# Kernel tuning notes

Measured on AMD Instinct MI355X. Metric: run time of the kernel, lower is better.

The kernel has to match this reference:

```python
import jax, jax.numpy as jnp
import numpy as np

Q = 3  # q_order: SelfONN concatenates powers x^1..x^Q on channel dim

def selfonn_conv(x, w, b, pad):
    # x: (B, C, H, W); w: (O, C*Q, kh, kw); b: (O,)
    xp = jnp.concatenate([x ** (i + 1) for i in range(Q)], axis=1)
    y = jax.lax.conv_general_dilated(
        xp, w, window_strides=(1, 1), padding=[(pad, pad), (pad, pad)],
        dimension_numbers=("NCHW", "OIHW", "NCHW"))
    return y + b[None, :, None, None]

def setup_inputs() -> dict:
    key = jax.random.key(0)
    ks = jax.random.split(key, 9)
    B, C, H, W = 4, 64, 64, 64
    P = 64  # pab_channels
    s1 = 1.0 / np.sqrt(C * Q)          # 1x1 convs
    s3 = 1.0 / np.sqrt(C * Q * 9)      # 3x3 convs
    return {
        "x": jax.random.normal(ks[0], (B, C, H, W), jnp.float32),
        "top_w": jax.random.normal(ks[1], (P, C * Q, 1, 1), jnp.float32) * s1,
        "top_b": jnp.zeros((P,), jnp.float32),
        "center_w": jax.random.normal(ks[2], (P, C * Q, 1, 1), jnp.float32) * s1,
        "center_b": jnp.zeros((P,), jnp.float32),
        "bottom_w": jax.random.normal(ks[3], (C, C * Q, 3, 3), jnp.float32) * s3,
        "bottom_b": jnp.zeros((C,), jnp.float32),
        "out_w": jax.random.normal(ks[4], (C, C * Q, 3, 3), jnp.float32) * s3,
        "out_b": jnp.zeros((C,), jnp.float32),
    }

def reference(x, top_w, top_b, center_w, center_b, bottom_w, bottom_b, out_w, out_b):
    B, C, H, W = x.shape
    HW = H * W
    x_top = selfonn_conv(x, top_w, top_b, 0).reshape(B, -1, HW)            # (B, P, HW)
    x_center = selfonn_conv(x, center_w, center_b, 0).reshape(B, -1, HW)  # (B, P, HW)
    x_bottom = selfonn_conv(x, bottom_w, bottom_b, 1).reshape(B, C, HW)   # (B, C, HW)
    x_center = jnp.swapaxes(x_center, 1, 2)  # (B, HW, P)
    x_bottom = jnp.swapaxes(x_bottom, 1, 2)  # (B, HW, C)
    sp = jnp.einsum("bnp,bpm->bnm", x_center, x_top)  # (B, HW, HW)
    # GLOBAL softmax over the entire HW*HW map per sample (dim=1 on flattened view)
    sp = jax.nn.softmax(sp.reshape(B, -1), axis=1).reshape(B, HW, HW)
    sp = jnp.einsum("bnm,bmc->bnc", sp, x_bottom)  # (B, HW, C)
    # faithful to torch: raw reshape (B, HW, C) -> (B, C, H, W), no transpose
    sp = sp.reshape(B, C, H, W)
    return selfonn_conv(x + sp, out_w, out_b, 1)
```

## Files before the change

### kernel.cpp

```cpp
#include <hip/hip_runtime.h>
#include <hip/hip_bf16.h>

namespace {
constexpr int IMG    = 262144;
constexpr int MS     = 4;
constexpr int PADIMG = 4356;
constexpr float LOG2E = 1.44269504088896340736f;
constexpr int WBFO  = 0;
constexpr int XPADO = 122880;
constexpr int TOPO  = 1795584;
constexpr int CENO  = 2319872;
constexpr int BOTO  = 2844160;
constexpr int PVO   = 3368448;
constexpr int MSO   = 5465600;
constexpr int ZSO   = 5467648;
}

using half8v  = __attribute__((ext_vector_type(8))) _Float16;
using half4v  = __attribute__((ext_vector_type(4))) _Float16;
using short8v = __attribute__((ext_vector_type(8))) short;
typedef __attribute__((ext_vector_type(4))) float f32x4;

__device__ __forceinline__ short f2bf(float f) {
    __hip_bfloat16 h = __float2bfloat16(f);
    return *reinterpret_cast<short*>(&h);
}
__device__ __forceinline__ float bf2f(short s) {
    unsigned u = ((unsigned)(unsigned short)s) << 16;
    return __uint_as_float(u);
}

__global__ __launch_bounds__(256) void k_prep(const float* __restrict__ bw, const float* __restrict__ ow,
                                              const float* __restrict__ tw, const float* __restrict__ cw,
                                              _Float16* __restrict__ wbf,
                                              const float* __restrict__ x, _Float16* __restrict__ xpad) {
    __shared__ float xs[64 * 65];
    int bx = blockIdx.x, t = threadIdx.x;
    if (bx < 960) {
        int idx = bx * 256 + t;
        if (idx < 221184) {
            int tsel = idx / 110592;
            int r    = idx - tsel * 110592;
            int tap  = r / 12288;
            int rr   = r - tap * 12288;
            int ck   = rr / 2048;
            int r2   = rr - ck * 2048;
            int o    = r2 >> 5;
            int ki   = r2 & 31;
            int k    = ck * 32 + ki;
            int p    = k >> 6, ci = k & 63;
            const float* src = tsel ? ow : bw;
            wbf[idx] = (_Float16)src[o * 1728 + (p * 64 + ci) * 9 + tap];
        } else {
            int j = idx - 221184;
            int tsel = j / 12288;
            int rr   = j - tsel * 12288;
            int ck   = rr / 2048;
            int r2   = rr - ck * 2048;
            int o    = r2 >> 5;
            int ki   = r2 & 31;
            int k    = ck * 32 + ki;
            wbf[idx] = (_Float16)(tsel ? cw[o * 192 + k] * LOG2E : tw[o * 192 + k]);
        }
        return;
    }
    int bx2 = bx - 960;
    int b = bx2 >> 6, h = bx2 & 63;
    {
        _Float16* base = xpad + (size_t)b * 6 * PADIMG * 32;
        int px[6];
        px[0] = (h + 1) * 66;
        px[1] = (h + 1) * 66 + 65;
        px[2] = h;
        px[3] = 65 * 66 + h;
        int npx = 4;
        if (h < 2) { px[4] = 64 + h; px[5] = 65 * 66 + 64 + h; npx = 6; }
        int pi = t / 24, ck = t % 24;
        if (pi < npx) {
            int cp = ck >> 2, q = ck & 3;
            half8v z = {0, 0, 0, 0, 0, 0, 0, 0};
            *(half8v*)&base[((size_t)cp * PADIMG + px[pi]) * 32 + q * 8] = z;
        }
    }
    #pragma unroll
    for (int it = 0; it < 16; ++it) {
        int idx = it * 256 + t;
        int ci = idx >> 6, wc = idx & 63;
        xs[ci * 65 + wc] = x[b * IMG + ci * 4096 + h * 64 + wc];
    }
    __syncthreads();
    _Float16* dst = xpad + ((size_t)b * 6 * PADIMG + (h + 1) * 66 + 1) * 32;
    #pragma unroll
    for (int it = 0; it < 6; ++it) {
        int u = it * 256 + t;
        int ck = u >> 8, within = u & 255;
        int px = within >> 2, q = within & 3;
        int k0 = ck * 32 + q * 8;
        int p = k0 >> 6, c0 = k0 & 63;
        half8v o;
        #pragma unroll
        for (int j = 0; j < 8; ++j) {
            float v = xs[(c0 + j) * 65 + px];
            float pw = (p == 0) ? v : ((p == 1) ? v * v : v * v * v);
            o[j] = (_Float16)pw;
        }
        *(half8v*)&dst[((size_t)ck * PADIMG + px) * 32 + q * 8] = o;
    }
}

__device__ __forceinline__ void conv3d32(int bx, int t,
                                         const _Float16* __restrict__ src,
                                         const _Float16* __restrict__ wt,
                                         const float* __restrict__ bias,
                                         _Float16* __restrict__ dh_, float* __restrict__ df) {
    int lane = t & 63, w = t >> 6;
    int l16 = lane & 15, quad = lane >> 4;
    int oh = bx >> 8, mt = bx & 255;
    int b = mt >> 6, h = mt & 63;
    const _Float16* abase = src + ((size_t)b * 6 * PADIMG + (h + 1) * 66 + 1 + w * 16 + l16) * 32 + quad * 8;
    const _Float16* bbase = wt + (size_t)(oh * 32 + l16) * 32 + quad * 8;
    f32x4 acc[2];
    acc[0] = (f32x4){0.f, 0.f, 0.f, 0.f};
    acc[1] = (f32x4){0.f, 0.f, 0.f, 0.f};
    for (int tap = 0; tap < 9; ++tap) {
        int dh = tap / 3 - 1, dw = tap % 3 - 1;
        const _Float16* arow = abase + (dh * 66 + dw) * 32;
        const _Float16* brow = bbase + (size_t)tap * 6 * 2048;
        #pragma unroll
        for (int c6 = 0; c6 < 6; ++c6) {
            half8v afr  = *(const half8v*)&arow[(size_t)c6 * PADIMG * 32];
            half8v bfr0 = *(const half8v*)&brow[(size_t)c6 * 2048];
            half8v bfr1 = *(const half8v*)&brow[(size_t)c6 * 2048 + 512];
            acc[0] = __builtin_amdgcn_mfma_f32_16x16x32_f16(afr, bfr0, acc[0], 0, 0, 0);
            acc[1] = __builtin_amdgcn_mfma_f32_16x16x32_f16(afr, bfr1, acc[1], 0, 0, 0);
        }
    }
    #pragma unroll
    for (int nf = 0; nf < 2; ++nf) {
        int c = oh * 32 + nf * 16 + l16;
        float bv = bias[c];
        size_t oi = (size_t)b * 262144 + (size_t)c * 4096 + h * 64 + w * 16 + quad * 4;
        if (dh_) {
            half4v o;
            #pragma unroll
            for (int r = 0; r < 4; ++r) o[r] = (_Float16)(acc[nf][r] + bv);
            *(half4v*)&dh_[oi] = o;
        } else {
            float4 o = make_float4(acc[nf][0] + bv, acc[nf][1] + bv, acc[nf][2] + bv, acc[nf][3] + bv);
            *(float4*)&df[oi] = o;
        }
    }
}

__global__ __launch_bounds__(256) void k_convs(const _Float16* __restrict__ xpad,
                                               const _Float16* __restrict__ wbf,
                                               const float* __restrict__ tb, const float* __restrict__ cb,
                                               const float* __restrict__ bbias,
                                               _Float16* __restrict__ topd, _Float16* __restrict__ cend,
                                               _Float16* __restrict__ botb) {
    int bx = blockIdx.x, t = threadIdx.x;
    if (bx < 512) {
        conv3d32(bx, t, xpad, wbf , bbias, botb, nullptr);
        return;
    }
    int bx2 = bx - 512;
    int lane = t & 63, w = t >> 6;
    int l16 = lane & 15, quad = lane >> 4;
    int ot = bx2 >> 8, mt = bx2 & 255;
    int b = mt >> 6, h = mt & 63;
    const _Float16* wt   = wbf + (ot ? 233472 : 221184);
    const float*    bias = ot ? cb : tb;
    _Float16*       dst  = (ot ? cend : topd) + (size_t)b * IMG;
    const _Float16* abase = xpad + ((size_t)b * 6 * PADIMG + (h + 1) * 66 + 1 + w * 16 + l16) * 32 + quad * 8;
    const _Float16* bbase = wt + (size_t)l16 * 32 + quad * 8;
    f32x4 acc[4];
    #pragma unroll
    for (int nf = 0; nf < 4; ++nf) acc[nf] = (f32x4){0.f, 0.f, 0.f, 0.f};
    #pragma unroll
    for (int kc = 0; kc < 6; ++kc) {
        half8v afr = *(const half8v*)&abase[(size_t)kc * PADIMG * 32];
        #pragma unroll
        for (int nf = 0; nf < 4; ++nf) {
            half8v bfr = *(const half8v*)&bbase[(size_t)kc * 2048 + nf * 16 * 32];
            acc[nf] = __builtin_amdgcn_mfma_f32_16x16x32_f16(afr, bfr, acc[nf], 0, 0, 0);
        }
    }
    _Float16* dp = dst + (size_t)(h * 64 + w * 16) * 64;
    #pragma unroll
    for (int nf = 0; nf < 4; ++nf) {
        float bv = bias[nf * 16 + l16];
        if (ot) bv *= LOG2E;
        #pragma unroll
        for (int r = 0; r < 4; ++r)
            dp[(quad * 4 + r) * 64 + nf * 16 + l16] = (_Float16)(acc[nf][r] + bv);
    }
}

__global__ __launch_bounds__(256) void k_attn(float* __restrict__ ws) {
    __shared__ _Float16 ltop[64 * 72];
    __shared__ _Float16 lbot[64 * 72];
    __shared__ _Float16 lp[128 * 72];
    int t    = threadIdx.x;
    int lane = t & 63, w = t >> 6;
    int l16  = lane & 15, quad = lane >> 4;
    int bx = blockIdx.x;
    int st = bx & 31, b = (bx >> 5) & 3, s = bx >> 7;
    int n0 = st * 128;
    const _Float16* topg = (const _Float16*)(ws + TOPO) + (size_t)b * IMG;
    const _Float16* ceng = (const _Float16*)(ws + CENO) + (size_t)b * IMG;
    const _Float16* botg = (const _Float16*)(ws + BOTO) + (size_t)b * IMG;

    half8v afr[2][2];
    #pragma unroll
    for (int i = 0; i < 2; ++i)
        #pragma unroll
        for (int kk = 0; kk < 2; ++kk)
            afr[i][kk] = *(const half8v*)&ceng[(size_t)(n0 + w * 32 + i * 16 + l16) * 64 + kk * 32 + quad * 8];

    int r0 = t >> 3, r1 = r0 + 32, off = (t & 7) * 8;
    int q2 = quad >> 1;
    int lpw = (w * 32 + quad * 4) * 72;
    int lpr = (w * 32 + l16) * 72;
    int rb3 = (l16 >> 3) & 1;

    f32x4 pv[2][4];
    #pragma unroll
    for (int i = 0; i < 2; ++i)
        #pragma unroll
        for (int j = 0; j < 4; ++j) pv[i][j] = (f32x4){0.f, 0.f, 0.f, 0.f};
    float runm = -3.0e38f, zacc = 0.f;

    int mp = s * 1024;
    half8v rt0 = *(const half8v*)&topg[(size_t)(mp + r0) * 64 + off];
    half8v rt1 = *(const half8v*)&topg[(size_t)(mp + r1) * 64 + off];
    half8v rb0 = *(const half8v*)&botg[(size_t)r0 * 4096 + mp + off];
    half8v rb1 = *(const half8v*)&botg[(size_t)r1 * 4096 + mp + off];

    for (int tt = 0; tt < 16; ++tt) {
        __syncthreads();
        *(half8v*)&ltop[r0 * 72 + off] = rt0;
        *(half8v*)&ltop[r1 * 72 + off] = rt1;
        *(half8v*)&lbot[r0 * 72 + off] = rb0;
        *(half8v*)&lbot[r1 * 72 + off] = rb1;
        __syncthreads();
        if (tt < 15) {
            int m1 = s * 1024 + (tt + 1) * 64;
            rt0 = *(const half8v*)&topg[(size_t)(m1 + r0) * 64 + off];
            rt1 = *(const half8v*)&topg[(size_t)(m1 + r1) * 64 + off];
            rb0 = *(const half8v*)&botg[(size_t)r0 * 4096 + m1 + off];
            rb1 = *(const half8v*)&botg[(size_t)r1 * 4096 + m1 + off];
        }
        f32x4 sa[2][4];
        #pragma unroll
        for (int i = 0; i < 2; ++i)
            #pragma unroll
            for (int j = 0; j < 4; ++j) sa[i][j] = (f32x4){0.f, 0.f, 0.f, 0.f};
        #pragma unroll
        for (int kk = 0; kk < 2; ++kk)
            #pragma unroll
            for (int j = 0; j < 4; ++j) {
                half8v bfr = *(half8v*)&ltop[(j * 16 + l16) * 72 + kk * 32 + quad * 8];
                sa[0][j] = __builtin_amdgcn_mfma_f32_16x16x32_f16(afr[0][kk], bfr, sa[0][j], 0, 0, 0);
                sa[1][j] = __builtin_amdgcn_mfma_f32_16x16x32_f16(afr[1][kk], bfr, sa[1][j], 0, 0, 0);
            }
        float tm = -3.0e38f;
        #pragma unroll
        for (int i = 0; i < 2; ++i)
            #pragma unroll
            for (int j = 0; j < 4; ++j)
                #pragma unroll
                for (int r = 0; r < 4; ++r) tm = fmaxf(tm, sa[i][j][r]);
        for (int o2 = 32; o2; o2 >>= 1) tm = fmaxf(tm, __shfl_xor(tm, o2, 64));
        float newm = fmaxf(runm, tm);
        if (newm > runm) {
            float sc = exp2f(runm - newm);
            zacc *= sc;
            #pragma unroll
            for (int i = 0; i < 2; ++i)
                #pragma unroll
                for (int j = 0; j < 4; ++j) pv[i][j] *= sc;
            runm = newm;
        }
        #pragma unroll
        for (int i = 0; i < 2; ++i)
            #pragma unroll
            for (int j = 0; j < 4; ++j) {
                int cb = (j ^ q2) * 16 + l16;
                #pragma unroll
                for (int r = 0; r < 4; ++r) {
                    float e = exp2f(sa[i][j][r] - runm);
                    zacc += e;
                    lp[lpw + i * 1152 + r * 72 + cb] = (_Float16)e;
                }
            }
        half8v pa[2][2];
        #pragma unroll
        for (int i = 0; i < 2; ++i)
            #pragma unroll
            for (int kk = 0; kk < 2; ++kk) {
                int jj = kk * 2 + q2;
                pa[i][kk] = *(half8v*)&lp[lpr + i * 1152 + ((jj ^ rb3) * 16) + (quad & 1) * 8];
            }
        #pragma unroll
        for (int kk = 0; kk < 2; ++kk)
            #pragma unroll
            for (int j = 0; j < 4; ++j) {
                half8v bb = *(half8v*)&lbot[(j * 16 + l16) * 72 + kk * 32 + quad * 8];
                pv[0][j] = __builtin_amdgcn_mfma_f32_16x16x32_f16(pa[0][kk], bb, pv[0][j], 0, 0, 0);
                pv[1][j] = __builtin_amdgcn_mfma_f32_16x16x32_f16(pa[1][kk], bb, pv[1][j], 0, 0, 0);
            }
    }
    for (int o2 = 32; o2; o2 >>= 1) zacc += __shfl_xor(zacc, o2, 64);
    if (lane == 0) {
        ws[MSO + s * 512 + b * 128 + st * 4 + w] = runm;
        ws[ZSO + s * 512 + b * 128 + st * 4 + w] = zacc;
    }
    short* pvp = (short*)(ws + PVO) + (size_t)s * 1048576 + (size_t)b * IMG;
    #pragma unroll
    for (int i = 0; i < 2; ++i)
        #pragma unroll
        for (int j = 0; j < 4; ++j)
            #pragma unroll
            for (int r = 0; r < 4; ++r)
                pvp[(size_t)(n0 + w * 32 + i * 16 + quad * 4 + r) * 64 + j * 16 + l16] = f2bf(pv[i][j][r]);
}

__global__ __launch_bounds__(256) void k_finalu(const float* __restrict__ x, float* __restrict__ ws,
                                                _Float16* __restrict__ upad) {
    __shared__ float us[64 * 65];
    __shared__ float rm[4], rz[4];
    int t = threadIdx.x, bx = blockIdx.x;
    int b = bx >> 6, h = bx & 63;
    int g = t & 127;
    float mv[4];
    float m = -3.0e38f;
    #pragma unroll
    for (int s = 0; s < 4; ++s) {
        mv[s] = ws[MSO + s * 512 + b * 128 + g];
        m = fmaxf(m, mv[s]);
    }
    for (int o2 = 32; o2; o2 >>= 1) m = fmaxf(m, __shfl_xor(m, o2, 64));
    if ((t & 63) == 0) rm[t >> 6] = m;
    __syncthreads();
    float M = fmaxf(fmaxf(rm[0], rm[1]), fmaxf(rm[2], rm[3]));
    float z = 0.f;
    if (t < 128) {
        #pragma unroll
        for (int s = 0; s < 4; ++s)
            z += ws[ZSO + s * 512 + b * 128 + g] * exp2f(mv[s] - M);
    }
    for (int o2 = 32; o2; o2 >>= 1) z += __shfl_xor(z, o2, 64);
    if ((t & 63) == 0) rz[t >> 6] = z;
    __syncthreads();
    float Z = rz[0] + rz[1] + rz[2] + rz[3];

    const short* pvb = (const short*)(ws + PVO) + (size_t)b * IMG;
    int hg = h >> 5;
    #pragma unroll
    for (int it = 0; it < 2; ++it) {
        int idx = it * 2048 + t * 8;
        int ci = idx >> 6, wc = idx & 63;
        int rem = ci * 4096 + h * 64 + wc;
        int grp = ci * 2 + hg;
        float acc[8] = {};
        #pragma unroll
        for (int s = 0; s < MS; ++s) {
            float scl = exp2f(ws[MSO + s * 512 + b * 128 + grp] - M);
            short8v pvv = *(const short8v*)&pvb[(size_t)s * 1048576 + rem];
            #pragma unroll
            for (int i = 0; i < 8; ++i) acc[i] += bf2f(pvv[i]) * scl;
        }
        float4 x0 = *(const float4*)&x[(size_t)b * IMG + rem];
        float4 x1 = *(const float4*)&x[(size_t)b * IMG + rem + 4];
        float xv[8] = {x0.x, x0.y, x0.z, x0.w, x1.x, x1.y, x1.z, x1.w};
        #pragma unroll
        for (int i = 0; i < 8; ++i)
            us[ci * 65 + wc + i] = xv[i] + acc[i] / Z;
    }
    __syncthreads();
    _Float16* dst = upad + ((size_t)b * 6 * PADIMG + (h + 1) * 66 + 1) * 32;
    #pragma unroll
    for (int it = 0; it < 6; ++it) {
        int u = it * 256 + t;
        int ck = u >> 8, within = u & 255;
        int px = within >> 2, q = within & 3;
        int k0 = ck * 32 + q * 8;
        int p = k0 >> 6, c0 = k0 & 63;
        half8v o;
        #pragma unroll
        for (int j = 0; j < 8; ++j) {
            float v = us[(c0 + j) * 65 + px];
            float pw = (p == 0) ? v : ((p == 1) ? v * v : v * v * v);
            o[j] = (_Float16)pw;
        }
        *(half8v*)&dst[((size_t)ck * PADIMG + px) * 32 + q * 8] = o;
    }
}

__global__ __launch_bounds__(256) void k_conv3o(const _Float16* __restrict__ upad,
                                                const _Float16* __restrict__ wout,
                                                const float* __restrict__ ob,
                                                float* __restrict__ out) {
    conv3d32(blockIdx.x, threadIdx.x, upad, wout, ob, nullptr, out);
}

extern "C" void kernel_launch(void* const* d_in, const int* in_sizes, int n_in,
                              void* d_out, int out_size, void* d_ws, size_t ws_size,
                              hipStream_t stream) {
    (void)in_sizes; (void)n_in; (void)out_size; (void)ws_size;
    const float* x  = (const float*)d_in[0];
    const float* tw = (const float*)d_in[1];
    const float* tb = (const float*)d_in[2];
    const float* cw = (const float*)d_in[3];
    const float* cb = (const float*)d_in[4];
    const float* bw = (const float*)d_in[5];
    const float* bb = (const float*)d_in[6];
    const float* ow = (const float*)d_in[7];
    const float* ob = (const float*)d_in[8];
    float* ws  = (float*)d_ws;
    float* out = (float*)d_out;

    _Float16* wbf  = (_Float16*)(ws + WBFO);
    _Float16* wout = wbf + 110592;
    _Float16* xpad = (_Float16*)(ws + XPADO);
    _Float16* topb = (_Float16*)(ws + TOPO);
    _Float16* cenb = (_Float16*)(ws + CENO);
    _Float16* botb = (_Float16*)(ws + BOTO);

    hipLaunchKernelGGL(k_prep, dim3(1216), dim3(256), 0, stream, bw, ow, tw, cw, wbf, x, xpad);
    hipLaunchKernelGGL(k_convs, dim3(1024), dim3(256), 0, stream, xpad, wbf, tb, cb, bb, topb, cenb, botb);
    hipLaunchKernelGGL(k_attn, dim3(512), dim3(256), 0, stream, ws);
    hipLaunchKernelGGL(k_finalu, dim3(256), dim3(256), 0, stream, x, ws, xpad);
    hipLaunchKernelGGL(k_conv3o, dim3(512), dim3(256), 0, stream, xpad, wout, ob, out);
}
```

Baseline: 167.0 us.

## Split attention key range across up to 8 slices with grid swizzle and MFMA priority

Makes the number of key splits in the flash-style attention kernel a runtime parameter, raising it from 4 to 8 when the workspace is large enough. This doubles the attention grid to fill more CUs, at the cost of more partial results to merge. The attention block index is also swizzled across XCDs, MFMA sections are wrapped in s_setprio, and the libm exp2f calls are replaced with the hardware exp2 builtin. The finalize kernel moves to 512 threads to merge the extra partials and multiplies by a reciprocal instead of dividing.

```diff
diff --git a/kernel.cpp b/kernel.cpp
--- a/kernel.cpp
+++ b/kernel.cpp
@@ -3,7 +3,6 @@
 
 namespace {
 constexpr int IMG    = 262144;
-constexpr int MS     = 4;
 constexpr int PADIMG = 4356;
 constexpr float LOG2E = 1.44269504088896340736f;
 constexpr int WBFO  = 0;
@@ -12,8 +11,9 @@
 constexpr int CENO  = 2319872;
 constexpr int BOTO  = 2844160;
 constexpr int PVO   = 3368448;
-constexpr int MSO   = 5465600;
-constexpr int ZSO   = 5467648;
+constexpr int MSO4  = 5465600;
+constexpr int MSO8  = 7562752;
+constexpr size_t NEED8 = (size_t)(MSO8 + 8192) * 4;
 }
 
 using half8v  = __attribute__((ext_vector_type(8))) _Float16;
@@ -196,16 +196,18 @@
     }
 }
 
-__global__ __launch_bounds__(256) void k_attn(float* __restrict__ ws) {
+__global__ __launch_bounds__(256) void k_attn(float* __restrict__ ws, int mtiles, int msoOff, int zsoOff) {
     __shared__ _Float16 ltop[64 * 72];
     __shared__ _Float16 lbot[64 * 72];
     __shared__ _Float16 lp[128 * 72];
     int t    = threadIdx.x;
     int lane = t & 63, w = t >> 6;
     int l16  = lane & 15, quad = lane >> 4;
-    int bx = blockIdx.x;
+    int bxr = blockIdx.x;
+    int bx  = (bxr & 7) * ((int)gridDim.x >> 3) + (bxr >> 3);
     int st = bx & 31, b = (bx >> 5) & 3, s = bx >> 7;
     int n0 = st * 128;
+    int mbase = s * mtiles * 64;
     const _Float16* topg = (const _Float16*)(ws + TOPO) + (size_t)b * IMG;
     const _Float16* ceng = (const _Float16*)(ws + CENO) + (size_t)b * IMG;
     const _Float16* botg = (const _Float16*)(ws + BOTO) + (size_t)b * IMG;
@@ -230,21 +232,20 @@
         for (int j = 0; j < 4; ++j) pv[i][j] = (f32x4){0.f, 0.f, 0.f, 0.f};
     float runm = -3.0e38f, zacc = 0.f;
 
-    int mp = s * 1024;
-    half8v rt0 = *(const half8v*)&topg[(size_t)(mp + r0) * 64 + off];
-    half8v rt1 = *(const half8v*)&topg[(size_t)(mp + r1) * 64 + off];
-    half8v rb0 = *(const half8v*)&botg[(size_t)r0 * 4096 + mp + off];
-    half8v rb1 = *(const half8v*)&botg[(size_t)r1 * 4096 + mp + off];
-
-    for (int tt = 0; tt < 16; ++tt) {
+    half8v rt0 = *(const half8v*)&topg[(size_t)(mbase + r0) * 64 + off];
+    half8v rt1 = *(const half8v*)&topg[(size_t)(mbase + r1) * 64 + off];
+    half8v rb0 = *(const half8v*)&botg[(size_t)r0 * 4096 + mbase + off];
+    half8v rb1 = *(const half8v*)&botg[(size_t)r1 * 4096 + mbase + off];
+
+    for (int tt = 0; tt < mtiles; ++tt) {
         __syncthreads();
         *(half8v*)&ltop[r0 * 72 + off] = rt0;
         *(half8v*)&ltop[r1 * 72 + off] = rt1;
         *(half8v*)&lbot[r0 * 72 + off] = rb0;
         *(half8v*)&lbot[r1 * 72 + off] = rb1;
         __syncthreads();
-        if (tt < 15) {
-            int m1 = s * 1024 + (tt + 1) * 64;
+        if (tt < mtiles - 1) {
+            int m1 = mbase + (tt + 1) * 64;
             rt0 = *(const half8v*)&topg[(size_t)(m1 + r0) * 64 + off];
             rt1 = *(const half8v*)&topg[(size_t)(m1 + r1) * 64 + off];
             rb0 = *(const half8v*)&botg[(size_t)r0 * 4096 + m1 + off];
@@ -255,6 +256,7 @@
         for (int i = 0; i < 2; ++i)
             #pragma unroll
             for (int j = 0; j < 4; ++j) sa[i][j] = (f32x4){0.f, 0.f, 0.f, 0.f};
+        __builtin_amdgcn_s_setprio(1);
         #pragma unroll
         for (int kk = 0; kk < 2; ++kk)
             #pragma unroll
@@ -263,17 +265,20 @@
                 sa[0][j] = __builtin_amdgcn_mfma_f32_16x16x32_f16(afr[0][kk], bfr, sa[0][j], 0, 0, 0);
                 sa[1][j] = __builtin_amdgcn_mfma_f32_16x16x32_f16(afr[1][kk], bfr, sa[1][j], 0, 0, 0);
             }
+        __builtin_amdgcn_s_setprio(0);
         float tm = -3.0e38f;
         #pragma unroll
         for (int i = 0; i < 2; ++i)
             #pragma unroll
-            for (int j = 0; j < 4; ++j)
-                #pragma unroll
-                for (int r = 0; r < 4; ++r) tm = fmaxf(tm, sa[i][j][r]);
+            for (int j = 0; j < 4; ++j) {
+                float a = fmaxf(sa[i][j][0], sa[i][j][1]);
+                float c = fmaxf(sa[i][j][2], sa[i][j][3]);
+                tm = fmaxf(tm, fmaxf(a, c));
+            }
         for (int o2 = 32; o2; o2 >>= 1) tm = fmaxf(tm, __shfl_xor(tm, o2, 64));
         float newm = fmaxf(runm, tm);
         if (newm > runm) {
-            float sc = exp2f(runm - newm);
+            float sc = __builtin_amdgcn_exp2f(runm - newm);
             zacc *= sc;
             #pragma unroll
             for (int i = 0; i < 2; ++i)
@@ -288,7 +293,7 @@
                 int cb = (j ^ q2) * 16 + l16;
                 #pragma unroll
                 for (int r = 0; r < 4; ++r) {
-                    float e = exp2f(sa[i][j][r] - runm);
+                    float e = __builtin_amdgcn_exp2f(sa[i][j][r] - runm);
                     zacc += e;
                     lp[lpw + i * 1152 + r * 72 + cb] = (_Float16)e;
                 }
@@ -301,6 +306,7 @@
                 int jj = kk * 2 + q2;
                 pa[i][kk] = *(half8v*)&lp[lpr + i * 1152 + ((jj ^ rb3) * 16) + (quad & 1) * 8];
             }
+        __builtin_amdgcn_s_setprio(1);
         #pragma unroll
         for (int kk = 0; kk < 2; ++kk)
             #pragma unroll
@@ -309,11 +315,12 @@
                 pv[0][j] = __builtin_amdgcn_mfma_f32_16x16x32_f16(pa[0][kk], bb, pv[0][j], 0, 0, 0);
                 pv[1][j] = __builtin_amdgcn_mfma_f32_16x16x32_f16(pa[1][kk], bb, pv[1][j], 0, 0, 0);
             }
+        __builtin_amdgcn_s_setprio(0);
     }
     for (int o2 = 32; o2; o2 >>= 1) zacc += __shfl_xor(zacc, o2, 64);
     if (lane == 0) {
-        ws[MSO + s * 512 + b * 128 + st * 4 + w] = runm;
-        ws[ZSO + s * 512 + b * 128 + st * 4 + w] = zacc;
+        ws[msoOff + s * 512 + b * 128 + st * 4 + w] = runm;
+        ws[zsoOff + s * 512 + b * 128 + st * 4 + w] = zacc;
     }
     short* pvp = (short*)(ws + PVO) + (size_t)s * 1048576 + (size_t)b * IMG;
     #pragma unroll
@@ -325,47 +332,47 @@
                 pvp[(size_t)(n0 + w * 32 + i * 16 + quad * 4 + r) * 64 + j * 16 + l16] = f2bf(pv[i][j][r]);
 }
 
-__global__ __launch_bounds__(256) void k_finalu(const float* __restrict__ x, float* __restrict__ ws,
-                                                _Float16* __restrict__ upad) {
+__global__ __launch_bounds__(512) void k_finalu(const float* __restrict__ x, float* __restrict__ ws,
+                                                _Float16* __restrict__ upad,
+                                                int ms, int msoOff, int zsoOff) {
     __shared__ float us[64 * 65];
-    __shared__ float rm[4], rz[4];
+    __shared__ float rm[8], rz[8];
     int t = threadIdx.x, bx = blockIdx.x;
     int b = bx >> 6, h = bx & 63;
     int g = t & 127;
-    float mv[4];
     float m = -3.0e38f;
-    #pragma unroll
-    for (int s = 0; s < 4; ++s) {
-        mv[s] = ws[MSO + s * 512 + b * 128 + g];
-        m = fmaxf(m, mv[s]);
-    }
+    for (int s = 0; s < ms; ++s)
+        m = fmaxf(m, ws[msoOff + s * 512 + b * 128 + g]);
     for (int o2 = 32; o2; o2 >>= 1) m = fmaxf(m, __shfl_xor(m, o2, 64));
     if ((t & 63) == 0) rm[t >> 6] = m;
     __syncthreads();
-    float M = fmaxf(fmaxf(rm[0], rm[1]), fmaxf(rm[2], rm[3]));
+    float M = rm[0];
+    #pragma unroll
+    for (int j = 1; j < 8; ++j) M = fmaxf(M, rm[j]);
     float z = 0.f;
     if (t < 128) {
-        #pragma unroll
-        for (int s = 0; s < 4; ++s)
-            z += ws[ZSO + s * 512 + b * 128 + g] * exp2f(mv[s] - M);
+        for (int s = 0; s < ms; ++s)
+            z += ws[zsoOff + s * 512 + b * 128 + g] *
+                 __builtin_amdgcn_exp2f(ws[msoOff + s * 512 + b * 128 + g] - M);
     }
     for (int o2 = 32; o2; o2 >>= 1) z += __shfl_xor(z, o2, 64);
     if ((t & 63) == 0) rz[t >> 6] = z;
     __syncthreads();
-    float Z = rz[0] + rz[1] + rz[2] + rz[3];
+    float Z = 0.f;
+    #pragma unroll
+    for (int j = 0; j < 8; ++j) Z += rz[j];
+    float rZ = 1.0f / Z;
 
     const short* pvb = (const short*)(ws + PVO) + (size_t)b * IMG;
     int hg = h >> 5;
-    #pragma unroll
-    for (int it = 0; it < 2; ++it) {
-        int idx = it * 2048 + t * 8;
+    {
+        int idx = t * 8;
         int ci = idx >> 6, wc = idx & 63;
         int rem = ci * 4096 + h * 64 + wc;
         int grp = ci * 2 + hg;
         float acc[8] = {};
-        #pragma unroll
-        for (int s = 0; s < MS; ++s) {
-            float scl = exp2f(ws[MSO + s * 512 + b * 128 + grp] - M);
+        for (int s = 0; s < ms; ++s) {
+            float scl = __builtin_amdgcn_exp2f(ws[msoOff + s * 512 + b * 128 + grp] - M);
             short8v pvv = *(const short8v*)&pvb[(size_t)s * 1048576 + rem];
             #pragma unroll
             for (int i = 0; i < 8; ++i) acc[i] += bf2f(pvv[i]) * scl;
@@ -375,13 +382,13 @@
         float xv[8] = {x0.x, x0.y, x0.z, x0.w, x1.x, x1.y, x1.z, x1.w};
         #pragma unroll
         for (int i = 0; i < 8; ++i)
-            us[ci * 65 + wc + i] = xv[i] + acc[i] / Z;
+            us[ci * 65 + wc + i] = xv[i] + acc[i] * rZ;
     }
     __syncthreads();
     _Float16* dst = upad + ((size_t)b * 6 * PADIMG + (h + 1) * 66 + 1) * 32;
     #pragma unroll
-    for (int it = 0; it < 6; ++it) {
-        int u = it * 256 + t;
+    for (int it = 0; it < 3; ++it) {
+        int u = it * 512 + t;
         int ck = u >> 8, within = u & 255;
         int px = within >> 2, q = within & 3;
         int k0 = ck * 32 + q * 8;
@@ -407,7 +414,7 @@
 extern "C" void kernel_launch(void* const* d_in, const int* in_sizes, int n_in,
                               void* d_out, int out_size, void* d_ws, size_t ws_size,
                               hipStream_t stream) {
-    (void)in_sizes; (void)n_in; (void)out_size; (void)ws_size;
+    (void)in_sizes; (void)n_in; (void)out_size;
     const float* x  = (const float*)d_in[0];
     const float* tw = (const float*)d_in[1];
     const float* tb = (const float*)d_in[2];
@@ -427,9 +434,14 @@
     _Float16* cenb = (_Float16*)(ws + CENO);
     _Float16* botb = (_Float16*)(ws + BOTO);
 
+    int ms     = (ws_size >= NEED8) ? 8 : 4;
+    int mtiles = 64 / ms;
+    int msoOff = (ms == 8) ? MSO8 : MSO4;
+    int zsoOff = msoOff + ms * 512;
+
     hipLaunchKernelGGL(k_prep, dim3(1216), dim3(256), 0, stream, bw, ow, tw, cw, wbf, x, xpad);
     hipLaunchKernelGGL(k_convs, dim3(1024), dim3(256), 0, stream, xpad, wbf, tb, cb, bb, topb, cenb, botb);
-    hipLaunchKernelGGL(k_attn, dim3(512), dim3(256), 0, stream, ws);
-    hipLaunchKernelGGL(k_finalu, dim3(256), dim3(256), 0, stream, x, ws, xpad);
+    hipLaunchKernelGGL(k_attn, dim3(128 * ms), dim3(256), 0, stream, ws, mtiles, msoOff, zsoOff);
+    hipLaunchKernelGGL(k_finalu, dim3(256), dim3(512), 0, stream, x, ws, xpad, ms, msoOff, zsoOff);
     hipLaunchKernelGGL(k_conv3o, dim3(512), dim3(256), 0, stream, xpad, wout, ob, out);
 }
```

After: 168.7 us. Within noise of the previous version (+1.0%).
